# Kernel optimization log

Measured on AMD Instinct MI355X. Metric: run time of the kernel, lower is better.

## Reference

```python
import jax, jax.numpy as jnp
import numpy as np

N_OP, N_TASK, N_TENSOR, N_LINK = 4096, 64, 32768, 1024
N_PLACE = N_OP * N_TASK
NODE_H, EDGE_H = 64, 8
RAW_OP, RAW_TASK, RAW_E = 256, 64, 16
ETYPES = ['link', 'prev', 'succ', 'place', 'serve']
N_LAYERS = 6


def setup_inputs():
    key = jax.random.key(0)
    ks = jax.random.split(key, 20)
    f = jnp.float32
    def w(k, shape, fan_in):
        return jax.random.normal(k, shape, f) / np.sqrt(fan_in)
    return {
        'op_feats': jax.random.normal(ks[0], (N_OP, RAW_OP), f),
        'task_feats': jax.random.normal(ks[1], (N_TASK, RAW_TASK), f),
        'tensor_feats': jax.random.normal(ks[2], (N_TENSOR, RAW_E), f),
        'link_feats': jax.random.normal(ks[3], (N_LINK, RAW_E), f),
        'place_feats': jax.random.normal(ks[4], (N_PLACE, RAW_E), f),
        'prev_src': jax.random.randint(ks[5], (N_TENSOR,), 0, N_OP, jnp.int32),
        'prev_dst': jax.random.randint(ks[6], (N_TENSOR,), 0, N_OP, jnp.int32),
        'link_src': jax.random.randint(ks[7], (N_LINK,), 0, N_TASK, jnp.int32),
        'link_dst': jax.random.randint(ks[8], (N_LINK,), 0, N_TASK, jnp.int32),
        'op_W': w(ks[9], (RAW_OP, NODE_H), RAW_OP),
        'op_b': jnp.zeros((NODE_H,), f),
        'task_W': w(ks[10], (RAW_TASK, NODE_H), RAW_TASK),
        'task_b': jnp.zeros((NODE_H,), f),
        # 5 per-etype edge-trans Dense layers, all raw edge dim = RAW_E
        'eW': w(ks[11], (5, RAW_E, EDGE_H), RAW_E),
        'eb': jnp.zeros((5, EDGE_H), f),
        # GConv Dense per (etype, layer): input = NODE_H + EDGE_H = 72
        'gW': w(ks[12], (5, N_LAYERS, NODE_H + EDGE_H, NODE_H), NODE_H + EDGE_H),
        'gb': jnp.zeros((5, N_LAYERS, NODE_H), f),
        'final_W': w(ks[13], (NODE_H + EDGE_H + NODE_H, 1), NODE_H + EDGE_H + NODE_H),
        'final_b': jnp.zeros((1,), f),
    }


def _mean_agg(msgs, dst, num_segments):
    s = jax.ops.segment_sum(msgs, dst, num_segments=num_segments)
    cnt = jax.ops.segment_sum(jnp.ones((msgs.shape[0], 1), msgs.dtype), dst,
                              num_segments=num_segments)
    return s / jnp.maximum(cnt, 1.0)


def _forward(op_feats, task_feats, tensor_feats, link_feats, place_feats,
             op_W, op_b, task_W, task_b, eW, eb, gW, gb, final_W, final_b,
             prev_src, prev_dst, link_src, link_dst):
    elu = jax.nn.elu
    op = elu(op_feats @ op_W + op_b)      # [N_OP, 64]
    task = elu(task_feats @ task_W + task_b)  # [N_TASK, 64]

    raw_e = {'link': link_feats, 'prev': tensor_feats, 'succ': tensor_feats,
             'place': place_feats, 'serve': place_feats}
    ef = {et: elu(raw_e[et] @ eW[i] + eb[i]) for i, et in enumerate(ETYPES)}

    # place edges: complete bipartite, row-major by op (matches final reshape)
    place_src = jnp.repeat(jnp.arange(N_OP, dtype=jnp.int32), N_TASK)
    place_dst = jnp.tile(jnp.arange(N_TASK, dtype=jnp.int32), N_OP)

    # etype -> (src_idx, dst_idx, src_kind, dst_kind)
    topo = {
        'link':  (link_src, link_dst, 'task', 'task'),
        'prev':  (prev_src, prev_dst, 'op', 'op'),
        'succ':  (prev_dst, prev_src, 'op', 'op'),
        'place': (place_src, place_dst, 'op', 'task'),
        'serve': (place_dst, place_src, 'task', 'op'),
    }
    n_nodes = {'op': N_OP, 'task': N_TASK}

    for l in range(N_LAYERS):
        op_dst, task_dst = [], []
        for i, et in enumerate(ETYPES):
            sidx, didx, skind, dkind = topo[et]
            src = op if skind == 'op' else task
            # gather-concat-Dense per edge: [E, 72] @ [72, 64]
            m = jnp.concatenate([src[sidx], ef[et]], axis=1) @ gW[i, l] + gb[i, l]
            o = _mean_agg(m, didx, n_nodes[dkind])
            (op_dst if dkind == 'op' else task_dst).append(o)
        op = elu(op + sum(op_dst) / len(op_dst))
        task = elu(task + sum(task_dst) / len(task_dst))

    # final per-place-edge score: concat(src op, place edge feat, dst task)
    d = jnp.concatenate([op[place_src], ef['place'], task[place_dst]], axis=1)
    d = d @ final_W + final_b  # [N_PLACE, 1]
    return jnp.reshape(d[:, 0], (N_OP, N_TASK))


def reference(op_feats, task_feats, tensor_feats, link_feats, place_feats,
              prev_src, prev_dst, link_src, link_dst,
              op_W, op_b, task_W, task_b, eW, eb, gW, gb, final_W, final_b):
    return _forward(op_feats, task_feats, tensor_feats, link_feats, place_feats,
                    op_W, op_b, task_W, task_b, eW, eb, gW, gb, final_W, final_b,
                    prev_src, prev_dst, link_src, link_dst)
```

## Files before the change

kernel.cpp:

```cpp
#include <hip/hip_runtime.h>
#include <math.h>

#define NOP 4096
#define NTASK 64
#define NTENSOR 32768
#define NLINK 1024
#define NPLACE (NOP*NTASK)
#define CAP 64
#define NOPB 512

enum : int {
  O_CNT_PREV  = 0,
  O_CNT_SUCC  = O_CNT_PREV + NOP,
  O_CNT_LINK  = O_CNT_SUCC + NOP,
  O_SEF_PREV  = O_CNT_LINK + 64,
  O_SEF_SUCC  = O_SEF_PREV + NOP*8,
  O_SEF_LINK  = O_SEF_SUCC + NOP*8,
  O_SEF_PLACE = O_SEF_LINK + 64*8,
  O_SEF_SERVE = O_SEF_PLACE + 64*8,
  O_OP_A      = O_SEF_SERVE + NOP*8,
  O_OP_B      = O_OP_A + NOP*64,
  O_TASK_A    = O_OP_B + NOP*64,
  O_TASK_B    = O_TASK_A + 64*64,
  O_BPLACE    = O_TASK_B + 64*64,
  O_AOP       = O_BPLACE + NPLACE,
  O_CVEC      = O_AOP + NOP,
  O_MOPP      = O_CVEC + 64,
  O_MTPP      = O_MOPP + 2*512*64,
  O_SPLP      = O_MTPP + 2*4*64,
  O_CSRP_PREV = O_SPLP + 256*512,
  O_CSRP_SUCC = O_CSRP_PREV + NOP*CAP,
  O_CSRP_LINK = O_CSRP_SUCC + NOP*CAP,
  O_EFS_PREV  = O_CSRP_LINK + 64*CAP,
  O_EFS_SUCC  = O_EFS_PREV + NOP*CAP*8,
  O_EFS_LINK  = O_EFS_SUCC + NOP*CAP*8,
  O_TOTAL     = O_EFS_LINK + 64*CAP*8
};

__device__ __forceinline__ float elu1(float x) { return x > 0.f ? x : expm1f(x); }

__device__ __forceinline__ void fma4(float4& a, const float s, const float4 w) {
  a.x = fmaf(s, w.x, a.x);
  a.y = fmaf(s, w.y, a.y);
  a.z = fmaf(s, w.z, a.z);
  a.w = fmaf(s, w.w, a.w);
}

__global__ __launch_bounds__(256) void k_pre(
    const float* __restrict__ taskA, const float* __restrict__ taskW,
    const float* __restrict__ taskb, float* __restrict__ ws)
{
  const int tid = threadIdx.x;
  const int bid = blockIdx.x;
  if (bid > 0) {
    int* ib = (int*)ws;
    for (int i = (bid - 1)*1024 + tid*4; i < NOP*2 + 64; i += 8192) {
      ib[O_CNT_PREV + i+0] = 0;
      ib[O_CNT_PREV + i+1] = 0;
      ib[O_CNT_PREV + i+2] = 0;
      ib[O_CNT_PREV + i+3] = 0;
    }
    return;
  }
  __shared__ float sA[64*65];
  __shared__ float sW[64*64];
  __shared__ float4 red[256];
  for (int i = tid; i < 4096; i += 256) {
    const int t = i >> 6, k = i & 63;
    sA[t*65 + k] = taskA[i];
  }
  for (int i = tid*4; i < 4096; i += 1024)
    *(float4*)&sW[i] = *(const float4*)&taskW[i];
  __syncthreads();
  const int og = tid >> 4, hq = tid & 15, h0 = hq*4;
  float4 msum = make_float4(0.f,0.f,0.f,0.f);
  for (int tg = 0; tg < 4; ++tg) {
    const int t = tg*16 + og;
    float4 acc = *(const float4*)&taskb[h0];
    const float* a = &sA[t*65];
    for (int k = 0; k < 64; ++k)
      fma4(acc, a[k], *(const float4*)&sW[k*64 + h0]);
    acc.x = elu1(acc.x); acc.y = elu1(acc.y); acc.z = elu1(acc.z); acc.w = elu1(acc.w);
    *(float4*)&ws[O_TASK_A + t*64 + h0] = acc;
    msum.x += acc.x; msum.y += acc.y; msum.z += acc.z; msum.w += acc.w;
  }
  red[tid] = msum;
  __syncthreads();
  if (tid < 16) {
    float4 s = make_float4(0.f,0.f,0.f,0.f);
    for (int g = 0; g < 16; ++g) {
      float4 v = red[g*16 + tid];
      s.x += v.x; s.y += v.y; s.z += v.z; s.w += v.w;
    }
    *(float4*)&ws[O_MTPP + tid*4] = s;
  }
}

__global__ __launch_bounds__(256) void k_prep(
    const float* __restrict__ opA, const float* __restrict__ opW, const float* __restrict__ opb,
    const float* __restrict__ tensor_feats, const float* __restrict__ link_feats,
    const float* __restrict__ place_feats,
    const int* __restrict__ prev_src, const int* __restrict__ prev_dst,
    const int* __restrict__ link_src, const int* __restrict__ link_dst,
    const float* __restrict__ eW, const float* __restrict__ eb,
    const float* __restrict__ finalW, float* __restrict__ ws)
{
  __shared__ float smem[13376];
  const int tid = threadIdx.x;
  const int bid = blockIdx.x;
  int* ib = (int*)ws;
  if (bid < 256) {
    float* sW = smem;
    float* sA = smem + 8192;
    float4* red = (float4*)(smem + 12352);
    const int obase = bid * 16;
    for (int i = tid; i < 4096; i += 256) {
      const int o = i >> 8, k = i & 255;
      sA[o*260 + k] = opA[(size_t)(obase + o)*256 + k];
    }
    const int o = tid >> 4, hq = tid & 15, h0 = hq*4;
    float4 acc = *(const float4*)&opb[h0];
    for (int half = 0; half < 2; ++half) {
      __syncthreads();
      for (int i = tid*4; i < 8192; i += 1024)
        *(float4*)&sW[i] = *(const float4*)&opW[half*8192 + i];
      __syncthreads();
      const float* a = &sA[o*260 + half*128];
      for (int k = 0; k < 128; ++k)
        fma4(acc, a[k], *(const float4*)&sW[k*64 + h0]);
    }
    acc.x = elu1(acc.x); acc.y = elu1(acc.y); acc.z = elu1(acc.z); acc.w = elu1(acc.w);
    *(float4*)&ws[O_OP_A + (size_t)(obase + o)*64 + h0] = acc;
    red[tid] = acc;
    __syncthreads();
    if (tid < 16) {
      float4 s = make_float4(0.f,0.f,0.f,0.f);
      for (int g = 0; g < 16; ++g) {
        float4 v = red[g*16 + tid];
        s.x += v.x; s.y += v.y; s.z += v.z; s.w += v.w;
      }
      *(float4*)&ws[O_MOPP + bid*64 + tid*4] = s;
    }
  } else if (bid < 384) {
    float* sEW = smem;
    float* sEB = smem + 384;
    for (int i = tid; i < 384; i += 256) sEW[i] = eW[i];
    if (tid < 24) sEB[tid] = eb[tid];
    __syncthreads();
    const int e = (bid - 256)*256 + tid;
    float raw[16];
    *(float4*)&raw[0]  = *(const float4*)&tensor_feats[(size_t)e*16 + 0];
    *(float4*)&raw[4]  = *(const float4*)&tensor_feats[(size_t)e*16 + 4];
    *(float4*)&raw[8]  = *(const float4*)&tensor_feats[(size_t)e*16 + 8];
    *(float4*)&raw[12] = *(const float4*)&tensor_feats[(size_t)e*16 + 12];
    float efp[8], efs[8];
#pragma unroll
    for (int c = 0; c < 8; ++c) { efp[c] = sEB[8+c]; efs[c] = sEB[16+c]; }
#pragma unroll
    for (int k = 0; k < 16; ++k) {
      const float a = raw[k];
#pragma unroll
      for (int c = 0; c < 8; ++c) {
        efp[c] = fmaf(a, sEW[128 + k*8 + c], efp[c]);
        efs[c] = fmaf(a, sEW[256 + k*8 + c], efs[c]);
      }
    }
#pragma unroll
    for (int c = 0; c < 8; ++c) { efp[c] = elu1(efp[c]); efs[c] = elu1(efs[c]); }
    const int pd = prev_dst[e], ps = prev_src[e];
    {
      int pos = atomicAdd(&ib[O_CNT_PREV + pd], 1);
      if (pos >= 0 && pos < CAP) {
        ib[O_CSRP_PREV + pd*CAP + pos] = ps;
        float* dst = ws + O_EFS_PREV + ((size_t)pd*CAP + pos)*8;
        *(float4*)&dst[0] = make_float4(efp[0],efp[1],efp[2],efp[3]);
        *(float4*)&dst[4] = make_float4(efp[4],efp[5],efp[6],efp[7]);
      }
    }
    {
      int pos = atomicAdd(&ib[O_CNT_SUCC + ps], 1);
      if (pos >= 0 && pos < CAP) {
        ib[O_CSRP_SUCC + ps*CAP + pos] = pd;
        float* dst = ws + O_EFS_SUCC + ((size_t)ps*CAP + pos)*8;
        *(float4*)&dst[0] = make_float4(efs[0],efs[1],efs[2],efs[3]);
        *(float4*)&dst[4] = make_float4(efs[4],efs[5],efs[6],efs[7]);
      }
    }
    if (e < NLINK) {
      float rl[16];
      *(float4*)&rl[0]  = *(const float4*)&link_feats[(size_t)e*16 + 0];
      *(float4*)&rl[4]  = *(const float4*)&link_feats[(size_t)e*16 + 4];
      *(float4*)&rl[8]  = *(const float4*)&link_feats[(size_t)e*16 + 8];
      *(float4*)&rl[12] = *(const float4*)&link_feats[(size_t)e*16 + 12];
      float efl[8];
#pragma unroll
      for (int c = 0; c < 8; ++c) efl[c] = sEB[c];
#pragma unroll
      for (int k = 0; k < 16; ++k) {
        const float a = rl[k];
#pragma unroll
        for (int c = 0; c < 8; ++c) efl[c] = fmaf(a, sEW[k*8 + c], efl[c]);
      }
      const int ld = link_dst[e];
      int pos = atomicAdd(&ib[O_CNT_LINK + ld], 1);
      if (pos >= 0 && pos < CAP) {
        ib[O_CSRP_LINK + ld*CAP + pos] = link_src[e];
        float* dst = ws + O_EFS_LINK + ((size_t)ld*CAP + pos)*8;
        *(float4*)&dst[0] = make_float4(elu1(efl[0]),elu1(efl[1]),elu1(efl[2]),elu1(efl[3]));
        *(float4*)&dst[4] = make_float4(elu1(efl[4]),elu1(efl[5]),elu1(efl[6]),elu1(efl[7]));
      }
    }
  } else {
    float* sW3 = smem;
    float* sW4 = smem + 128;
    float* sB3 = smem + 256;
    float* sB4 = smem + 264;
    float* sW1 = smem + 272;
    float* pl  = smem + 280;
    const int pbid = bid - 384;
    if (tid < 128) { sW3[tid] = eW[3*128 + tid]; sW4[tid] = eW[4*128 + tid]; }
    if (tid < 8) { sB3[tid] = eb[24+tid]; sB4[tid] = eb[32+tid]; sW1[tid] = finalW[64+tid]; }
    for (int i = tid; i < 512; i += 256) pl[i] = 0.f;
    __syncthreads();
    const int lane = tid & 63;
    const int wave = (pbid*256 + tid) >> 6;
    float pacc[8];
#pragma unroll
    for (int c = 0; c < 8; ++c) pacc[c] = 0.f;
    float* bplace = ws + O_BPLACE;
    float* sserve = ws + O_SEF_SERVE;
    for (int j = 0; j < 4; ++j) {
      const int i = wave*4 + j;
      const int e = i*64 + lane;
      float raw[16];
      *(float4*)&raw[0]  = *(const float4*)&place_feats[(size_t)e*16 + 0];
      *(float4*)&raw[4]  = *(const float4*)&place_feats[(size_t)e*16 + 4];
      *(float4*)&raw[8]  = *(const float4*)&place_feats[(size_t)e*16 + 8];
      *(float4*)&raw[12] = *(const float4*)&place_feats[(size_t)e*16 + 12];
      float efp[8], efs[8];
#pragma unroll
      for (int c = 0; c < 8; ++c) { efp[c] = sB3[c]; efs[c] = sB4[c]; }
#pragma unroll
      for (int k = 0; k < 16; ++k) {
        const float a = raw[k];
#pragma unroll
        for (int c = 0; c < 8; ++c) {
          efp[c] = fmaf(a, sW3[k*8 + c], efp[c]);
          efs[c] = fmaf(a, sW4[k*8 + c], efs[c]);
        }
      }
      float bp = 0.f;
#pragma unroll
      for (int c = 0; c < 8; ++c) {
        efp[c] = elu1(efp[c]);
        efs[c] = elu1(efs[c]);
        bp = fmaf(efp[c], sW1[c], bp);
        pacc[c] += efp[c];
      }
      bplace[e] = bp;
#pragma unroll
      for (int c = 0; c < 8; ++c) {
        float v = efs[c];
        for (int m = 32; m >= 1; m >>= 1) v += __shfl_xor(v, m, 64);
        if (lane == 0) sserve[i*8 + c] = v;
      }
    }
#pragma unroll
    for (int c = 0; c < 8; ++c) atomicAdd(&pl[lane*8 + c], pacc[c]);
    __syncthreads();
    for (int i = tid; i < 512; i += 256) ws[O_SPLP + pbid*512 + i] = pl[i];
  }
}

__global__ __launch_bounds__(256) void k_layer(
    const int l,
    const float* __restrict__ gW, const float* __restrict__ gb,
    const float* __restrict__ finalW,
    const float* __restrict__ op_in, float* __restrict__ op_out,
    const float* __restrict__ task_in, float* __restrict__ task_out,
    float* __restrict__ ws)
{
  __shared__ float smem[12544];
  const int tid = threadIdx.x;
  const int bid = blockIdx.x;
  const int* ib = (const int*)ws;
  const int rpar = l & 1, wpar = 1 - rpar;

  if (bid < NOPB) {
    float* sWp    = smem;
    float* sWs    = smem + 4608;
    float* sWeS   = smem + 9216;
    float* vp     = smem + 9728;
    float* sums_p = smem + 9984;
    float* sums_s = smem + 10528;
    float* sGB    = smem + 11072;
    float* sef    = smem + 11200;
    float* mop    = smem + 11392;
    int* idxp_s   = (int*)(smem + 11456);
    int* idxs_s   = (int*)(smem + 11968);
    int* cp_s     = (int*)(smem + 12480);
    int* cs_s     = (int*)(smem + 12488);

    const int obase = bid*8;
    const float* gWprev  = gW + (size_t)((6  + l)*72)*64;
    const float* gWsucc  = gW + (size_t)((12 + l)*72)*64;
    const float* gWserve = gW + (size_t)((24 + l)*72)*64;

    float4 wreg[10];
#pragma unroll
    for (int j = 0; j < 10; ++j) {
      const int i = tid*4 + j*1024;
      if (i < 9728) {
        const float* src = (i < 4608) ? &gWprev[i]
                         : (i < 9216) ? &gWsucc[i - 4608]
                                      : &gWserve[4096 + (i - 9216)];
        wreg[j] = *(const float4*)src;
      }
    }
    if (tid < 8) cp_s[tid] = ib[O_CNT_PREV + obase + tid];
    else if (tid < 16) cs_s[tid-8] = ib[O_CNT_SUCC + obase + (tid-8)];
    for (int i = tid; i < 8*CAP; i += 256) {
      const int o = i >> 6, j = i & 63;
      if (j < ib[O_CNT_PREV + obase + o]) idxp_s[i] = ib[O_CSRP_PREV + (obase+o)*CAP + j];
      if (j < ib[O_CNT_SUCC + obase + o]) idxs_s[i] = ib[O_CSRP_SUCC + (obase+o)*CAP + j];
    }
    if (tid < 128) sGB[tid] = (tid < 64) ? gb[(6+l)*64 + tid] : gb[(12+l)*64 + (tid-64)];
    if (tid < 64) mop[tid] = 0.f;
    if (l == 0) {
      if (tid >= 128 && tid < 192) sef[tid] = ws[O_SEF_SERVE + obase*8 + (tid-128)];
    } else {
      if (tid < 64)       sef[tid] = ws[O_SEF_PREV + obase*8 + tid];
      else if (tid < 128) sef[tid] = ws[O_SEF_SUCC + obase*8 + (tid-64)];
      else if (tid < 192) sef[tid] = ws[O_SEF_SERVE + obase*8 + (tid-128)];
    }
    {
      const int col = tid & 63, g = tid >> 6;
      const float* mtpp = ws + O_MTPP + rpar*256;
      const int nst = (l == 0) ? 1 : 4;
      float acc = (g == 0) ? gb[(24+l)*64 + col] : 0.f;
      for (int kk = 0; kk < 16; ++kk) {
        const int k = g*16 + kk;
        float mt = 0.f;
        for (int s = 0; s < nst; ++s) mt += mtpp[s*64 + k];
        acc = fmaf(mt*(1.f/64.f), gWserve[k*64 + col], acc);
      }
      vp[g*64 + col] = acc;
    }
    __syncthreads();

    const int wv = tid >> 6, lane = tid & 63;
#pragma unroll
    for (int oo = 0; oo < 2; ++oo) {
      const int o = 2*wv + oo;
      const int pep = min(cp_s[o], CAP);
      const int pes = min(cs_s[o], CAP);
      const int* ip = &idxp_s[o*CAP];
      const int* iq = &idxs_s[o*CAP];
      float p0=0.f,p1=0.f,p2=0.f,p3=0.f,q0=0.f,q1=0.f,q2=0.f,q3=0.f;
      int p = 0, q = 0;
      while (p+3 < pep && q+3 < pes) {
        const int a0=ip[p],a1=ip[p+1],a2=ip[p+2],a3=ip[p+3];
        const int b0=iq[q],b1=iq[q+1],b2=iq[q+2],b3=iq[q+3];
        p0 += op_in[(size_t)a0*64 + lane];
        p1 += op_in[(size_t)a1*64 + lane];
        p2 += op_in[(size_t)a2*64 + lane];
        p3 += op_in[(size_t)a3*64 + lane];
        q0 += op_in[(size_t)b0*64 + lane];
        q1 += op_in[(size_t)b1*64 + lane];
        q2 += op_in[(size_t)b2*64 + lane];
        q3 += op_in[(size_t)b3*64 + lane];
        p += 4; q += 4;
      }
      for (; p+3 < pep; p += 4) {
        const int a0=ip[p],a1=ip[p+1],a2=ip[p+2],a3=ip[p+3];
        p0 += op_in[(size_t)a0*64 + lane];
        p1 += op_in[(size_t)a1*64 + lane];
        p2 += op_in[(size_t)a2*64 + lane];
        p3 += op_in[(size_t)a3*64 + lane];
      }
      for (; q+3 < pes; q += 4) {
        const int b0=iq[q],b1=iq[q+1],b2=iq[q+2],b3=iq[q+3];
        q0 += op_in[(size_t)b0*64 + lane];
        q1 += op_in[(size_t)b1*64 + lane];
        q2 += op_in[(size_t)b2*64 + lane];
        q3 += op_in[(size_t)b3*64 + lane];
      }
      for (; p < pep; ++p) p0 += op_in[(size_t)ip[p]*64 + lane];
      for (; q < pes; ++q) q0 += op_in[(size_t)iq[q]*64 + lane];
      sums_p[o*68 + lane] = (p0+p1)+(p2+p3);
      sums_s[o*68 + lane] = (q0+q1)+(q2+q3);
    }
    if (l == 0) {
      if (tid < 128) {
        const bool isP = (tid < 64);
        const int t2 = tid & 63;
        const int o = t2 >> 3, c = t2 & 7;
        const int cnt = min(isP ? cp_s[o] : cs_s[o], CAP);
        const float* efs = ws + (isP ? O_EFS_PREV : O_EFS_SUCC) + ((size_t)(obase+o)*CAP)*8;
        float s0=0.f,s1=0.f,s2=0.f,s3=0.f;
        int j = 0;
        for (; j+3 < cnt; j += 4) {
          s0 += efs[j*8+c]; s1 += efs[(j+1)*8+c];
          s2 += efs[(j+2)*8+c]; s3 += efs[(j+3)*8+c];
        }
        for (; j < cnt; ++j) s0 += efs[j*8+c];
        const float s = (s0+s1)+(s2+s3);
        sef[tid] = s;
        ws[(isP ? O_SEF_PREV : O_SEF_SUCC) + obase*8 + t2] = s;
      }
    }
#pragma unroll
    for (int j = 0; j < 10; ++j) {
      const int i = tid*4 + j*1024;
      if (i < 9728) *(float4*)&smem[i] = wreg[j];
    }
    __syncthreads();

    const int oL = tid >> 5, c = (tid & 31)*2;
    const int d  = obase + oL;
    float up0 = 0.f, up1 = 0.f, us0 = 0.f, us1 = 0.f;
    const int cp = cp_s[oL];
    if (cp > 0) {
      float a0 = 0.f, a1 = 0.f;
      for (int k = 0; k < 64; ++k) {
        const float sk = sums_p[oL*68 + k];
        const float2 wv2 = *(const float2*)&sWp[k*64 + c];
        a0 = fmaf(sk, wv2.x, a0);
        a1 = fmaf(sk, wv2.y, a1);
      }
#pragma unroll
      for (int cc = 0; cc < 8; ++cc) {
        const float ev = sef[oL*8 + cc];
        const float2 wv2 = *(const float2*)&sWp[4096 + cc*64 + c];
        a0 = fmaf(ev, wv2.x, a0);
        a1 = fmaf(ev, wv2.y, a1);
      }
      const float r = 1.f/(float)cp;
      up0 = fmaf(a0, r, sGB[c]);
      up1 = fmaf(a1, r, sGB[c+1]);
    }
    const int cs = cs_s[oL];
    if (cs > 0) {
      float a0 = 0.f, a1 = 0.f;
      for (int k = 0; k < 64; ++k) {
        const float sk = sums_s[oL*68 + k];
        const float2 wv2 = *(const float2*)&sWs[k*64 + c];
        a0 = fmaf(sk, wv2.x, a0);
        a1 = fmaf(sk, wv2.y, a1);
      }
#pragma unroll
      for (int cc = 0; cc < 8; ++cc) {
        const float ev = sef[64 + oL*8 + cc];
        const float2 wv2 = *(const float2*)&sWs[4096 + cc*64 + c];
        a0 = fmaf(ev, wv2.x, a0);
        a1 = fmaf(ev, wv2.y, a1);
      }
      const float r = 1.f/(float)cs;
      us0 = fmaf(a0, r, sGB[64 + c]);
      us1 = fmaf(a1, r, sGB[64 + c + 1]);
    }
    float g0, g1;
    {
      const float2 v0 = *(const float2*)&vp[c];
      const float2 v1 = *(const float2*)&vp[64 + c];
      const float2 v2 = *(const float2*)&vp[128 + c];
      const float2 v3 = *(const float2*)&vp[192 + c];
      g0 = (v0.x + v1.x) + (v2.x + v3.x);
      g1 = (v0.y + v1.y) + (v2.y + v3.y);
#pragma unroll
      for (int cc = 0; cc < 8; ++cc) {
        const float ev = sef[128 + oL*8 + cc] * (1.f/64.f);
        const float2 wv2 = *(const float2*)&sWeS[cc*64 + c];
        g0 = fmaf(ev, wv2.x, g0);
        g1 = fmaf(ev, wv2.y, g1);
      }
    }
    const float2 x = *(const float2*)&op_in[(size_t)d*64 + c];
    const float r0 = elu1(x.x + (up0 + us0 + g0)*(1.f/3.f));
    const float r1 = elu1(x.y + (up1 + us1 + g1)*(1.f/3.f));
    if (l < 5) {
      float2 xo; xo.x = r0; xo.y = r1;
      *(float2*)&op_out[(size_t)d*64 + c] = xo;
      atomicAdd(&mop[c],   r0);
      atomicAdd(&mop[c+1], r1);
      __syncthreads();
      if (tid < 64) ws[O_MOPP + wpar*32768 + bid*64 + tid] = mop[tid];
    } else {
      float av = r0*finalW[c] + r1*finalW[c+1];
      av += __shfl_xor(av, 1, 64);
      av += __shfl_xor(av, 2, 64);
      av += __shfl_xor(av, 4, 64);
      av += __shfl_xor(av, 8, 64);
      av += __shfl_xor(av, 16, 64);
      if ((tid & 31) == 0) ws[O_AOP + d] = av;
    }
  } else {
    const int tbase = (bid - NOPB)*16;
    float* sTask  = smem;
    float* sW0    = smem + 4096;
    float* sWe3   = smem + 8704;
    float* vpl    = smem + 9216;
    float* mo4    = smem + 9472;
    float* sums_l = smem + 9728;
    float* sGB0   = smem + 10816;
    float* sefl   = smem + 10880;
    float* sefpl  = smem + 11008;
    float* mtp    = smem + 11136;
    int* idxl_s   = (int*)(smem + 11200);
    int* cl_s     = (int*)(smem + 12224);

    const float* gWlink  = gW + (size_t)(l*72)*64;
    const float* gWplace = gW + (size_t)((18 + l)*72)*64;

    {
      const int col = tid & 63, g = tid >> 6;
      const float* mopp = ws + O_MOPP + rpar*32768;
      const int nso = (l == 0) ? 256 : 512;
      float a0=0.f,a1=0.f,a2=0.f,a3=0.f,a4=0.f,a5=0.f,a6=0.f,a7=0.f;
      for (int s = g; s < nso; s += 32) {
        a0 += mopp[(s+0 )*64 + col];
        a1 += mopp[(s+4 )*64 + col];
        a2 += mopp[(s+8 )*64 + col];
        a3 += mopp[(s+12)*64 + col];
        a4 += mopp[(s+16)*64 + col];
        a5 += mopp[(s+20)*64 + col];
        a6 += mopp[(s+24)*64 + col];
        a7 += mopp[(s+28)*64 + col];
      }
      mo4[g*64 + col] = ((a0+a1)+(a2+a3)) + ((a4+a5)+(a6+a7));
    }
    for (int i = tid*4; i < 4096; i += 1024)
      *(float4*)&sTask[i] = *(const float4*)&task_in[i];
    for (int i = tid*4; i < 4608; i += 1024)
      *(float4*)&sW0[i] = *(const float4*)&gWlink[i];
    if (tid*4 < 512) *(float4*)&sWe3[tid*4] = *(const float4*)&gWplace[4096 + tid*4];
    if (tid < 16) cl_s[tid] = ib[O_CNT_LINK + tbase + tid];
    for (int i = tid; i < 16*CAP; i += 256) {
      const int t = i >> 6, j = i & 63;
      if (j < ib[O_CNT_LINK + tbase + t]) idxl_s[i] = ib[O_CSRP_LINK + (tbase+t)*CAP + j];
    }
    if (tid < 64) { sGB0[tid] = gb[l*64 + tid]; mtp[tid] = 0.f; }
    if (l == 0) {
      if (tid < 128) {
        const int t = tid >> 3, c = tid & 7;
        const int cnt = min(ib[O_CNT_LINK + tbase + t], CAP);
        const float* efs = ws + O_EFS_LINK + ((size_t)(tbase+t)*CAP)*8;
        float s0 = 0.f, s1 = 0.f;
        int j = 0;
        for (; j+1 < cnt; j += 2) { s0 += efs[j*8+c]; s1 += efs[j*8+8+c]; }
        if (j < cnt) s0 += efs[j*8+c];
        const float s = s0 + s1;
        sefl[tid] = s;
        ws[O_SEF_LINK + tbase*8 + tid] = s;
      } else {
        const int idx = tid - 128;
        float s0=0.f,s1=0.f,s2=0.f,s3=0.f;
        for (int r = 0; r < 256; r += 4) {
          s0 += ws[O_SPLP + (r+0)*512 + tbase*8 + idx];
          s1 += ws[O_SPLP + (r+1)*512 + tbase*8 + idx];
          s2 += ws[O_SPLP + (r+2)*512 + tbase*8 + idx];
          s3 += ws[O_SPLP + (r+3)*512 + tbase*8 + idx];
        }
        const float s = (s0+s1)+(s2+s3);
        sefpl[idx] = s;
        ws[O_SEF_PLACE + tbase*8 + idx] = s;
      }
    } else {
      if (tid < 128) sefl[tid] = ws[O_SEF_LINK + tbase*8 + tid];
      else sefpl[tid - 128] = ws[O_SEF_PLACE + tbase*8 + (tid - 128)];
    }
    __syncthreads();
    {
      const int col = tid & 63, g = tid >> 6;
      float acc = (g == 0) ? gb[(18+l)*64 + col] : 0.f;
      for (int kk = 0; kk < 16; ++kk) {
        const int k = g*16 + kk;
        const float mok = (mo4[k] + mo4[64+k]) + (mo4[128+k] + mo4[192+k]);
        acc = fmaf(mok*(1.f/4096.f), gWplace[k*64 + col], acc);
      }
      vpl[g*64 + col] = acc;
    }
    __syncthreads();

    const int wv = tid >> 6, lane = tid & 63;
#pragma unroll
    for (int tt = 0; tt < 4; ++tt) {
      const int t = 4*wv + tt;
      const int pe = min(cl_s[t], CAP);
      float s0=0.f,s1=0.f,s2=0.f,s3=0.f;
      int p = 0;
      for (; p+3 < pe; p += 4) {
        s0 += sTask[idxl_s[t*CAP+p  ]*64 + lane];
        s1 += sTask[idxl_s[t*CAP+p+1]*64 + lane];
        s2 += sTask[idxl_s[t*CAP+p+2]*64 + lane];
        s3 += sTask[idxl_s[t*CAP+p+3]*64 + lane];
      }
      for (; p < pe; ++p) s0 += sTask[idxl_s[t*CAP+p]*64 + lane];
      sums_l[t*68 + lane] = (s0+s1)+(s2+s3);
    }

    const int tL = tid >> 4, h0 = (tid & 15)*4;
    const int tG = tbase + tL;
    float4 ul = make_float4(0.f,0.f,0.f,0.f);
    const int cl2 = cl_s[tL];
    if (cl2 > 0) {
      float4 a = make_float4(0.f,0.f,0.f,0.f);
      for (int k = 0; k < 64; ++k)
        fma4(a, sums_l[tL*68 + k], *(const float4*)&sW0[k*64 + h0]);
#pragma unroll
      for (int cc = 0; cc < 8; ++cc)
        fma4(a, sefl[tL*8 + cc], *(const float4*)&sW0[4096 + cc*64 + h0]);
      const float r = 1.f/(float)cl2;
      ul.x = fmaf(a.x, r, sGB0[h0+0]);
      ul.y = fmaf(a.y, r, sGB0[h0+1]);
      ul.z = fmaf(a.z, r, sGB0[h0+2]);
      ul.w = fmaf(a.w, r, sGB0[h0+3]);
    }
    float4 uq;
    {
      const float4 v0 = *(const float4*)&vpl[h0];
      const float4 v1 = *(const float4*)&vpl[64 + h0];
      const float4 v2 = *(const float4*)&vpl[128 + h0];
      const float4 v3 = *(const float4*)&vpl[192 + h0];
      uq.x = (v0.x+v1.x)+(v2.x+v3.x);
      uq.y = (v0.y+v1.y)+(v2.y+v3.y);
      uq.z = (v0.z+v1.z)+(v2.z+v3.z);
      uq.w = (v0.w+v1.w)+(v2.w+v3.w);
#pragma unroll
      for (int cc = 0; cc < 8; ++cc)
        fma4(uq, sefpl[tL*8 + cc]*(1.f/4096.f), *(const float4*)&sWe3[cc*64 + h0]);
    }
    float4 x = *(const float4*)&sTask[tG*64 + h0];
    x.x = elu1(x.x + (ul.x + uq.x)*0.5f);
    x.y = elu1(x.y + (ul.y + uq.y)*0.5f);
    x.z = elu1(x.z + (ul.z + uq.z)*0.5f);
    x.w = elu1(x.w + (ul.w + uq.w)*0.5f);
    if (l < 5) {
      *(float4*)&task_out[(size_t)tG*64 + h0] = x;
      atomicAdd(&mtp[h0+0], x.x);
      atomicAdd(&mtp[h0+1], x.y);
      atomicAdd(&mtp[h0+2], x.z);
      atomicAdd(&mtp[h0+3], x.w);
      __syncthreads();
      if (tid < 64) ws[O_MTPP + wpar*256 + (bid - NOPB)*64 + tid] = mtp[tid];
    } else {
      const float4 fw = *(const float4*)&finalW[72 + h0];
      float cv = x.x*fw.x + x.y*fw.y + x.z*fw.z + x.w*fw.w;
      cv += __shfl_xor(cv, 1, 64);
      cv += __shfl_xor(cv, 2, 64);
      cv += __shfl_xor(cv, 4, 64);
      cv += __shfl_xor(cv, 8, 64);
      if ((tid & 15) == 0) ws[O_CVEC + tG] = cv;
    }
  }
}

__global__ __launch_bounds__(256) void k_final(
    const float* __restrict__ ws, const float* __restrict__ finalb,
    float* __restrict__ out)
{
  const int e4 = (blockIdx.x*256 + threadIdx.x)*4;
  const int i = e4 >> 6;
  const int t = e4 & 63;
  const float a = ws[O_AOP + i];
  const float fb = finalb[0];
  const float4 bp = *(const float4*)&ws[O_BPLACE + e4];
  const float4 cv = *(const float4*)&ws[O_CVEC + t];
  float4 o4;
  o4.x = a + bp.x + cv.x + fb;
  o4.y = a + bp.y + cv.y + fb;
  o4.z = a + bp.z + cv.z + fb;
  o4.w = a + bp.w + cv.w + fb;
  *(float4*)&out[e4] = o4;
}

extern "C" void kernel_launch(void* const* d_in, const int* in_sizes, int n_in,
                              void* d_out, int out_size, void* d_ws, size_t ws_size,
                              hipStream_t stream)
{
  (void)in_sizes; (void)n_in; (void)out_size;
  if (ws_size < (size_t)O_TOTAL * sizeof(float)) return;

  const float* op_feats     = (const float*)d_in[0];
  const float* task_feats   = (const float*)d_in[1];
  const float* tensor_feats = (const float*)d_in[2];
  const float* link_feats   = (const float*)d_in[3];
  const float* place_feats  = (const float*)d_in[4];
  const int*   prev_src     = (const int*)d_in[5];
  const int*   prev_dst     = (const int*)d_in[6];
  const int*   link_src     = (const int*)d_in[7];
  const int*   link_dst     = (const int*)d_in[8];
  const float* op_W         = (const float*)d_in[9];
  const float* op_b         = (const float*)d_in[10];
  const float* task_W       = (const float*)d_in[11];
  const float* task_b       = (const float*)d_in[12];
  const float* eW           = (const float*)d_in[13];
  const float* eb           = (const float*)d_in[14];
  const float* gW           = (const float*)d_in[15];
  const float* gb           = (const float*)d_in[16];
  const float* finalW       = (const float*)d_in[17];
  const float* finalb       = (const float*)d_in[18];
  float* w = (float*)d_ws;
  float* out = (float*)d_out;

  k_pre<<<9, 256, 0, stream>>>(task_feats, task_W, task_b, w);
  k_prep<<<640, 256, 0, stream>>>(op_feats, op_W, op_b,
                                  tensor_feats, link_feats, place_feats,
                                  prev_src, prev_dst, link_src, link_dst,
                                  eW, eb, finalW, w);

  for (int l = 0; l < 6; ++l) {
    const float* oin  = w + ((l & 1) ? O_OP_B : O_OP_A);
    float*       oout = w + ((l & 1) ? O_OP_A : O_OP_B);
    const float* tin  = w + ((l & 1) ? O_TASK_B : O_TASK_A);
    float*       tout = w + ((l & 1) ? O_TASK_A : O_TASK_B);
    k_layer<<<NOPB + 4, 256, 0, stream>>>(l, gW, gb, finalW, oin, oout, tin, tout, w);
  }

  k_final<<<256, 256, 0, stream>>>(w, finalb, out);
}
```

Measured before the change: 222.2 us.

## Split prep into embed and edge/place kernels, store layer weights directly to shared memory

Moves the op embedding matmul out of the edge/place prep kernel into a new embed kernel, alongside the task embedding and counter zeroing. This shrinks shared memory in the edge/place kernel from about 53KB to about 3KB, so more blocks can be resident. The op embedding now stages weights in four 64-row chunks to use less shared memory. In the layer kernel, gW is copied straight into shared memory instead of being held in 10 float4 registers across the CSR loads, which reduces register pressure but gives up some overlap of load latency.

New measurement: 196.6 us, median of 2. 1.13x faster.

```diff
diff --git a/kernel.cpp b/kernel.cpp
--- a/kernel.cpp
+++ b/kernel.cpp
@@ -46,58 +46,85 @@
   a.w = fmaf(s, w.w, a.w);
 }
 
-__global__ __launch_bounds__(256) void k_pre(
-    const float* __restrict__ taskA, const float* __restrict__ taskW,
-    const float* __restrict__ taskb, float* __restrict__ ws)
+__global__ __launch_bounds__(256) void k_embed(
+    const float* __restrict__ opA, const float* __restrict__ opW, const float* __restrict__ opb,
+    const float* __restrict__ taskA, const float* __restrict__ taskW, const float* __restrict__ taskb,
+    float* __restrict__ ws)
 {
+  __shared__ float smem[9280];
   const int tid = threadIdx.x;
   const int bid = blockIdx.x;
-  if (bid > 0) {
+  if (bid < 256) {
+    float* sW = smem;
+    float* sA = smem + 4096;
+    float4* red = (float4*)(smem + 8256);
+    const int obase = bid * 16;
+    for (int i = tid; i < 4096; i += 256) {
+      const int o = i >> 8, k = i & 255;
+      sA[o*260 + k] = opA[(size_t)(obase + o)*256 + k];
+    }
+    const int o = tid >> 4, hq = tid & 15, h0 = hq*4;
+    float4 acc = *(const float4*)&opb[h0];
+    for (int q = 0; q < 4; ++q) {
+      __syncthreads();
+      for (int i = tid*4; i < 4096; i += 1024)
+        *(float4*)&sW[i] = *(const float4*)&opW[q*4096 + i];
+      __syncthreads();
+      const float* a = &sA[o*260 + q*64];
+      for (int k = 0; k < 64; ++k)
+        fma4(acc, a[k], *(const float4*)&sW[k*64 + h0]);
+    }
+    acc.x = elu1(acc.x); acc.y = elu1(acc.y); acc.z = elu1(acc.z); acc.w = elu1(acc.w);
+    *(float4*)&ws[O_OP_A + (size_t)(obase + o)*64 + h0] = acc;
+    red[tid] = acc;
+    __syncthreads();
+    if (tid < 16) {
+      float4 s = make_float4(0.f,0.f,0.f,0.f);
+      for (int g = 0; g < 16; ++g) {
+        float4 v = red[g*16 + tid];
+        s.x += v.x; s.y += v.y; s.z += v.z; s.w += v.w;
+      }
+      *(float4*)&ws[O_MOPP + bid*64 + tid*4] = s;
+    }
+  } else {
+    float* sA = smem;
+    float* sW = smem + 4160;
+    float4* red = (float4*)(smem + 8256);
     int* ib = (int*)ws;
-    for (int i = (bid - 1)*1024 + tid*4; i < NOP*2 + 64; i += 8192) {
-      ib[O_CNT_PREV + i+0] = 0;
-      ib[O_CNT_PREV + i+1] = 0;
-      ib[O_CNT_PREV + i+2] = 0;
-      ib[O_CNT_PREV + i+3] = 0;
-    }
-    return;
-  }
-  __shared__ float sA[64*65];
-  __shared__ float sW[64*64];
-  __shared__ float4 red[256];
-  for (int i = tid; i < 4096; i += 256) {
-    const int t = i >> 6, k = i & 63;
-    sA[t*65 + k] = taskA[i];
-  }
-  for (int i = tid*4; i < 4096; i += 1024)
-    *(float4*)&sW[i] = *(const float4*)&taskW[i];
-  __syncthreads();
-  const int og = tid >> 4, hq = tid & 15, h0 = hq*4;
-  float4 msum = make_float4(0.f,0.f,0.f,0.f);
-  for (int tg = 0; tg < 4; ++tg) {
-    const int t = tg*16 + og;
-    float4 acc = *(const float4*)&taskb[h0];
-    const float* a = &sA[t*65];
-    for (int k = 0; k < 64; ++k)
-      fma4(acc, a[k], *(const float4*)&sW[k*64 + h0]);
-    acc.x = elu1(acc.x); acc.y = elu1(acc.y); acc.z = elu1(acc.z); acc.w = elu1(acc.w);
-    *(float4*)&ws[O_TASK_A + t*64 + h0] = acc;
-    msum.x += acc.x; msum.y += acc.y; msum.z += acc.z; msum.w += acc.w;
-  }
-  red[tid] = msum;
-  __syncthreads();
-  if (tid < 16) {
-    float4 s = make_float4(0.f,0.f,0.f,0.f);
-    for (int g = 0; g < 16; ++g) {
-      float4 v = red[g*16 + tid];
-      s.x += v.x; s.y += v.y; s.z += v.z; s.w += v.w;
-    }
-    *(float4*)&ws[O_MTPP + tid*4] = s;
+    for (int i = tid; i < NOP*2 + 64; i += 256) ib[O_CNT_PREV + i] = 0;
+    for (int i = tid; i < 4096; i += 256) {
+      const int t = i >> 6, k = i & 63;
+      sA[t*65 + k] = taskA[i];
+    }
+    for (int i = tid*4; i < 4096; i += 1024)
+      *(float4*)&sW[i] = *(const float4*)&taskW[i];
+    __syncthreads();
+    const int og = tid >> 4, hq = tid & 15, h0 = hq*4;
+    float4 msum = make_float4(0.f,0.f,0.f,0.f);
+    for (int tg = 0; tg < 4; ++tg) {
+      const int t = tg*16 + og;
+      float4 acc = *(const float4*)&taskb[h0];
+      const float* a = &sA[t*65];
+      for (int k = 0; k < 64; ++k)
+        fma4(acc, a[k], *(const float4*)&sW[k*64 + h0]);
+      acc.x = elu1(acc.x); acc.y = elu1(acc.y); acc.z = elu1(acc.z); acc.w = elu1(acc.w);
+      *(float4*)&ws[O_TASK_A + t*64 + h0] = acc;
+      msum.x += acc.x; msum.y += acc.y; msum.z += acc.z; msum.w += acc.w;
+    }
+    red[tid] = msum;
+    __syncthreads();
+    if (tid < 16) {
+      float4 s = make_float4(0.f,0.f,0.f,0.f);
+      for (int g = 0; g < 16; ++g) {
+        float4 v = red[g*16 + tid];
+        s.x += v.x; s.y += v.y; s.z += v.z; s.w += v.w;
+      }
+      *(float4*)&ws[O_MTPP + tid*4] = s;
+    }
   }
 }
 
-__global__ __launch_bounds__(256) void k_prep(
-    const float* __restrict__ opA, const float* __restrict__ opW, const float* __restrict__ opb,
+__global__ __launch_bounds__(256) void k_edge_place(
     const float* __restrict__ tensor_feats, const float* __restrict__ link_feats,
     const float* __restrict__ place_feats,
     const int* __restrict__ prev_src, const int* __restrict__ prev_dst,
@@ -105,49 +132,17 @@
     const float* __restrict__ eW, const float* __restrict__ eb,
     const float* __restrict__ finalW, float* __restrict__ ws)
 {
-  __shared__ float smem[13376];
+  __shared__ float smem[792];
   const int tid = threadIdx.x;
   const int bid = blockIdx.x;
   int* ib = (int*)ws;
-  if (bid < 256) {
-    float* sW = smem;
-    float* sA = smem + 8192;
-    float4* red = (float4*)(smem + 12352);
-    const int obase = bid * 16;
-    for (int i = tid; i < 4096; i += 256) {
-      const int o = i >> 8, k = i & 255;
-      sA[o*260 + k] = opA[(size_t)(obase + o)*256 + k];
-    }
-    const int o = tid >> 4, hq = tid & 15, h0 = hq*4;
-    float4 acc = *(const float4*)&opb[h0];
-    for (int half = 0; half < 2; ++half) {
-      __syncthreads();
-      for (int i = tid*4; i < 8192; i += 1024)
-        *(float4*)&sW[i] = *(const float4*)&opW[half*8192 + i];
-      __syncthreads();
-      const float* a = &sA[o*260 + half*128];
-      for (int k = 0; k < 128; ++k)
-        fma4(acc, a[k], *(const float4*)&sW[k*64 + h0]);
-    }
-    acc.x = elu1(acc.x); acc.y = elu1(acc.y); acc.z = elu1(acc.z); acc.w = elu1(acc.w);
-    *(float4*)&ws[O_OP_A + (size_t)(obase + o)*64 + h0] = acc;
-    red[tid] = acc;
-    __syncthreads();
-    if (tid < 16) {
-      float4 s = make_float4(0.f,0.f,0.f,0.f);
-      for (int g = 0; g < 16; ++g) {
-        float4 v = red[g*16 + tid];
-        s.x += v.x; s.y += v.y; s.z += v.z; s.w += v.w;
-      }
-      *(float4*)&ws[O_MOPP + bid*64 + tid*4] = s;
-    }
-  } else if (bid < 384) {
+  if (bid < 128) {
     float* sEW = smem;
     float* sEB = smem + 384;
     for (int i = tid; i < 384; i += 256) sEW[i] = eW[i];
     if (tid < 24) sEB[tid] = eb[tid];
     __syncthreads();
-    const int e = (bid - 256)*256 + tid;
+    const int e = bid*256 + tid;
     float raw[16];
     *(float4*)&raw[0]  = *(const float4*)&tensor_feats[(size_t)e*16 + 0];
     *(float4*)&raw[4]  = *(const float4*)&tensor_feats[(size_t)e*16 + 4];
@@ -170,7 +165,7 @@
     const int pd = prev_dst[e], ps = prev_src[e];
     {
       int pos = atomicAdd(&ib[O_CNT_PREV + pd], 1);
-      if (pos >= 0 && pos < CAP) {
+      if (pos < CAP) {
         ib[O_CSRP_PREV + pd*CAP + pos] = ps;
         float* dst = ws + O_EFS_PREV + ((size_t)pd*CAP + pos)*8;
         *(float4*)&dst[0] = make_float4(efp[0],efp[1],efp[2],efp[3]);
@@ -179,7 +174,7 @@
     }
     {
       int pos = atomicAdd(&ib[O_CNT_SUCC + ps], 1);
-      if (pos >= 0 && pos < CAP) {
+      if (pos < CAP) {
         ib[O_CSRP_SUCC + ps*CAP + pos] = pd;
         float* dst = ws + O_EFS_SUCC + ((size_t)ps*CAP + pos)*8;
         *(float4*)&dst[0] = make_float4(efs[0],efs[1],efs[2],efs[3]);
@@ -203,7 +198,7 @@
       }
       const int ld = link_dst[e];
       int pos = atomicAdd(&ib[O_CNT_LINK + ld], 1);
-      if (pos >= 0 && pos < CAP) {
+      if (pos < CAP) {
         ib[O_CSRP_LINK + ld*CAP + pos] = link_src[e];
         float* dst = ws + O_EFS_LINK + ((size_t)ld*CAP + pos)*8;
         *(float4*)&dst[0] = make_float4(elu1(efl[0]),elu1(efl[1]),elu1(efl[2]),elu1(efl[3]));
@@ -217,7 +212,7 @@
     float* sB4 = smem + 264;
     float* sW1 = smem + 272;
     float* pl  = smem + 280;
-    const int pbid = bid - 384;
+    const int pbid = bid - 128;
     if (tid < 128) { sW3[tid] = eW[3*128 + tid]; sW4[tid] = eW[4*128 + tid]; }
     if (tid < 8) { sB3[tid] = eb[24+tid]; sB4[tid] = eb[32+tid]; sW1[tid] = finalW[64+tid]; }
     for (int i = tid; i < 512; i += 256) pl[i] = 0.f;
@@ -306,17 +301,11 @@
     const float* gWsucc  = gW + (size_t)((12 + l)*72)*64;
     const float* gWserve = gW + (size_t)((24 + l)*72)*64;
 
-    float4 wreg[10];
-#pragma unroll
-    for (int j = 0; j < 10; ++j) {
-      const int i = tid*4 + j*1024;
-      if (i < 9728) {
-        const float* src = (i < 4608) ? &gWprev[i]
-                         : (i < 9216) ? &gWsucc[i - 4608]
-                                      : &gWserve[4096 + (i - 9216)];
-        wreg[j] = *(const float4*)src;
-      }
-    }
+    for (int i = tid*4; i < 4608; i += 1024) {
+      *(float4*)&sWp[i] = *(const float4*)&gWprev[i];
+      *(float4*)&sWs[i] = *(const float4*)&gWsucc[i];
+    }
+    if (tid*4 < 512) *(float4*)&sWeS[tid*4] = *(const float4*)&gWserve[4096 + tid*4];
     if (tid < 8) cp_s[tid] = ib[O_CNT_PREV + obase + tid];
     else if (tid < 16) cs_s[tid-8] = ib[O_CNT_SUCC + obase + (tid-8)];
     for (int i = tid; i < 8*CAP; i += 256) {
@@ -408,11 +397,6 @@
         sef[tid] = s;
         ws[(isP ? O_SEF_PREV : O_SEF_SUCC) + obase*8 + t2] = s;
       }
-    }
-#pragma unroll
-    for (int j = 0; j < 10; ++j) {
-      const int i = tid*4 + j*1024;
-      if (i < 9728) *(float4*)&smem[i] = wreg[j];
     }
     __syncthreads();
 
@@ -703,11 +687,10 @@
   float* w = (float*)d_ws;
   float* out = (float*)d_out;
 
-  k_pre<<<9, 256, 0, stream>>>(task_feats, task_W, task_b, w);
-  k_prep<<<640, 256, 0, stream>>>(op_feats, op_W, op_b,
-                                  tensor_feats, link_feats, place_feats,
-                                  prev_src, prev_dst, link_src, link_dst,
-                                  eW, eb, finalW, w);
+  k_embed<<<257, 256, 0, stream>>>(op_feats, op_W, op_b, task_feats, task_W, task_b, w);
+  k_edge_place<<<384, 256, 0, stream>>>(tensor_feats, link_feats, place_feats,
+                                        prev_src, prev_dst, link_src, link_dst,
+                                        eW, eb, finalW, w);
 
   for (int l = 0; l < 6; ++l) {
     const float* oin  = w + ((l & 1) ? O_OP_B : O_OP_A);
```
